# Kernel optimization log

Hardware: AMD Instinct MI355X
Metric: run time of the kernel (lower is better)

The kernel has to match this reference:

```python
import jax, jax.numpy as jnp
import numpy as np

N = 100000
E = 1600000
NFEAT = 128
NHID1 = 128
NHID2 = 128
NCLASS = 40


def setup_inputs() -> dict:
    key = jax.random.key(0)
    ks = jax.random.split(key, 16)
    x = jax.random.normal(ks[0], (N, NFEAT), dtype=jnp.float32)
    src = jax.random.randint(ks[1], (E,), 0, N, dtype=jnp.int32)
    dst = jax.random.randint(ks[2], (E,), 0, N, dtype=jnp.int32)
    s = 0.05
    params = {
        # SAGE layer 1: self branch and neighbor branch
        'w1s': jax.random.normal(ks[3], (NFEAT, NHID1), dtype=jnp.float32) * s,
        'b1s': jnp.zeros((NHID1,), dtype=jnp.float32),
        'w1n': jax.random.normal(ks[4], (NFEAT, NHID1), dtype=jnp.float32) * s,
        'b1n': jnp.zeros((NHID1,), dtype=jnp.float32),
        # SAGE layer 2 (input dim 2*NHID1)
        'w2s': jax.random.normal(ks[5], (2 * NHID1, NHID2), dtype=jnp.float32) * s,
        'b2s': jnp.zeros((NHID2,), dtype=jnp.float32),
        'w2n': jax.random.normal(ks[6], (2 * NHID1, NHID2), dtype=jnp.float32) * s,
        'b2n': jnp.zeros((NHID2,), dtype=jnp.float32),
        # final linear head (input dim 2*NHID2)
        'wfc': jax.random.normal(ks[7], (2 * NHID2, NCLASS), dtype=jnp.float32) * s,
        'bfc': jnp.zeros((NCLASS,), dtype=jnp.float32),
    }
    return {'x': x, 'src': src, 'dst': dst, **params}


def _neigh_mean(h, src, dst, n_nodes):
    # mean aggregation == spmm(row-normalized adj, h), via segment sum over edges
    msg = jax.ops.segment_sum(h[src], dst, num_segments=n_nodes)  # [N, d]
    cnt = jax.ops.segment_sum(jnp.ones((src.shape[0],), h.dtype), dst, num_segments=n_nodes)
    return msg / jnp.maximum(cnt, 1.0)[:, None]


def _sage_layer(h, src, dst, ws, bs, wn, bn):
    neigh = _neigh_mean(h, src, dst, h.shape[0])
    return jnp.concatenate([h @ ws + bs, neigh @ wn + bn], axis=1)


def _l2_normalize(h, eps=1e-12):
    nrm = jnp.sqrt(jnp.sum(h * h, axis=1, keepdims=True))
    return h / jnp.maximum(nrm, eps)


def reference(x, src, dst, w1s, b1s, w1n, b1n, w2s, b2s, w2n, b2n, wfc, bfc):
    h = jax.nn.relu(_sage_layer(x, src, dst, w1s, b1s, w1n, b1n))  # [N, 2*NHID1]
    h = _l2_normalize(h)
    # dropout is identity in eval mode
    h = jax.nn.relu(_sage_layer(h, src, dst, w2s, b2s, w2n, b2n))  # [N, 2*NHID2]
    h = _l2_normalize(h)
    return h @ wfc + bfc  # [N, NCLASS]
```

## Files before the change

### kernel.cpp

```cpp
#include <hip/hip_runtime.h>
#include <hip/hip_bf16.h>


#define N_NODES 100000
#define N_EDGES 1600000
#define NBUCK   196
#define BCAP    12288
#define CHUNK   4096

typedef unsigned short u16;
typedef __bf16 bf16x8 __attribute__((ext_vector_type(8)));
typedef float  f32x4  __attribute__((ext_vector_type(4)));

__device__ __forceinline__ u16 f2b(float f) {
  unsigned x = __builtin_bit_cast(unsigned, f);
  unsigned r = x + 0x7fffu + ((x >> 16) & 1u);
  return (u16)(r >> 16);
}
__device__ __forceinline__ float b2f(u16 u) {
  return __builtin_bit_cast(float, (unsigned)u << 16);
}
__device__ __forceinline__ bf16x8 ldfrag(const u16* p) {
  uint4 u = *reinterpret_cast<const uint4*>(p);
  return __builtin_bit_cast(bf16x8, u);
}

__global__ __launch_bounds__(256) void prep_weights(
    const float* __restrict__ w1s, const float* __restrict__ w1n,
    const float* __restrict__ w2s, const float* __restrict__ w2n,
    const float* __restrict__ wfc,
    u16* __restrict__ WT1, u16* __restrict__ WT2, u16* __restrict__ WFCT) {
  int i = blockIdx.x * 256 + threadIdx.x;
  if (i < 32768) {
    int c = i >> 7, k = i & 127;
    float v = (c < 128) ? w1s[k * 128 + c] : w1n[k * 128 + (c - 128)];
    WT1[c * 128 + k] = f2b(v);
  } else if (i < 32768 + 65536) {
    int j = i - 32768;
    int c = j >> 8, k = j & 255;
    float v = (c < 128) ? w2s[k * 128 + c] : w2n[k * 128 + (c - 128)];
    WT2[c * 256 + k] = f2b(v);
  } else {
    int j = i - 98304;
    int c = j >> 8, k = j & 255;
    float v = (c < 40) ? wfc[k * 40 + c] : 0.f;
    WFCT[c * 256 + k] = f2b(v);
  }
}

__global__ __launch_bounds__(256) void cvt_bf16(const float* __restrict__ x,
                                                u16* __restrict__ xb) {
  size_t i = ((size_t)blockIdx.x * 256 + threadIdx.x) * 8;
  float4 a = *reinterpret_cast<const float4*>(x + i);
  float4 b = *reinterpret_cast<const float4*>(x + i + 4);
  u16 o[8] = {f2b(a.x), f2b(a.y), f2b(a.z), f2b(a.w),
              f2b(b.x), f2b(b.y), f2b(b.z), f2b(b.w)};
  *reinterpret_cast<uint4*>(xb + i) = *reinterpret_cast<const uint4*>(o);
}

__device__ __forceinline__ int wave_incl_scan(int x, int lane) {
#pragma unroll
  for (int d = 1; d < 64; d <<= 1) {
    int n = __shfl_up(x, d, 64);
    if (lane >= d) x += n;
  }
  return x;
}

__global__ __launch_bounds__(256) void bucket_kernel(
    const int* __restrict__ src, const int* __restrict__ dst,
    int* __restrict__ cntg, uint2* __restrict__ pairBuf) {
  __shared__ unsigned hist[NBUCK];
  __shared__ unsigned gbase[NBUCK];
  __shared__ int sws[4];
  __shared__ uint2 stage[CHUNK];
  __shared__ int tgt[CHUNK];
  const int tid = threadIdx.x, lane = tid & 63, wid = tid >> 6;
  const int e0 = blockIdx.x * CHUNK;

  for (int i = tid; i < NBUCK; i += 256) hist[i] = 0u;
  __syncthreads();

  unsigned myD[16], myS[16];
  int myR[16], myB[16];
#pragma unroll
  for (int k = 0; k < 16; ++k) {
    int e = e0 + k * 256 + tid;
    if (e < N_EDGES) {
      unsigned d = (unsigned)dst[e];
      myD[k] = d;
      myS[k] = (unsigned)src[e];
      myB[k] = (int)(d >> 9);
      myR[k] = (int)atomicAdd(&hist[myB[k]], 1u);
    } else {
      myB[k] = -1;
    }
  }
  __syncthreads();

  int cnt = (tid < NBUCK) ? (int)hist[tid] : 0;
  int inc = wave_incl_scan(cnt, lane);
  if (lane == 63) sws[wid] = inc;
  __syncthreads();
  if (wid == 0) {
    int s = (lane < 4) ? sws[lane] : 0;
    s = wave_incl_scan(s, lane);
    if (lane < 4) sws[lane] = s;
  }
  __syncthreads();
  int excl = (wid ? sws[wid - 1] : 0) + inc - cnt;
  int gofs = 0;
  if (tid < NBUCK && cnt > 0) gofs = tid * BCAP + atomicAdd(&cntg[tid], cnt);
  __syncthreads();
  if (tid < NBUCK) {
    hist[tid] = (unsigned)excl;
    gbase[tid] = (unsigned)gofs;
  }
  __syncthreads();

#pragma unroll
  for (int k = 0; k < 16; ++k) {
    if (myB[k] >= 0) {
      int slot = (int)hist[myB[k]] + myR[k];
      uint2 pr;
      pr.x = myD[k];
      pr.y = myS[k];
      stage[slot] = pr;
      tgt[slot] = (int)gbase[myB[k]] + myR[k];
    }
  }
  __syncthreads();
  int nvalid = N_EDGES - e0;
  if (nvalid > CHUNK) nvalid = CHUNK;
  for (int i = tid; i < nvalid; i += 256) pairBuf[tgt[i]] = stage[i];
}

__global__ __launch_bounds__(256) void k_ebase(const int* __restrict__ cntg,
                                               int* __restrict__ ebase) {
  const int tid = threadIdx.x, lane = tid & 63, wid = tid >> 6;
  __shared__ int sws[4];
  int v = (tid < NBUCK) ? cntg[tid] : 0;
  int inc = wave_incl_scan(v, lane);
  if (lane == 63) sws[wid] = inc;
  __syncthreads();
  if (wid == 0) {
    int s = (lane < 4) ? sws[lane] : 0;
    s = wave_incl_scan(s, lane);
    if (lane < 4) sws[lane] = s;
  }
  __syncthreads();
  if (tid < NBUCK) ebase[tid] = (wid ? sws[wid - 1] : 0) + inc - v;
}

__global__ __launch_bounds__(512) void csr_build(
    const uint2* __restrict__ pairBuf, const int* __restrict__ cntg,
    const int* __restrict__ ebase, int* __restrict__ rowptr,
    int* __restrict__ csr) {
  __shared__ int lcnt[512];
  __shared__ int lofs[512];
  __shared__ int sws[8];
  __shared__ int cstage[10240];
  const int b = blockIdx.x, tid = threadIdx.x;
  const int lane = tid & 63, wid = tid >> 6;
  int nb = cntg[b];
  if (nb > BCAP) nb = BCAP;
  if (nb > 10240) nb = 10240;
  const int eb = ebase[b];
  const uint2* pp = pairBuf + (size_t)b * BCAP;

  lcnt[tid] = 0;
  __syncthreads();
  for (int i = tid; i < nb; i += 512) atomicAdd(&lcnt[pp[i].x & 511], 1);
  __syncthreads();
  int v = lcnt[tid];
  int inc = wave_incl_scan(v, lane);
  if (lane == 63) sws[wid] = inc;
  __syncthreads();
  if (wid == 0) {
    int s = (lane < 8) ? sws[lane] : 0;
    s = wave_incl_scan(s, lane);
    if (lane < 8) sws[lane] = s;
  }
  __syncthreads();
  int excl = (wid ? sws[wid - 1] : 0) + inc - v;
  int node = b * 512 + tid;
  if (node <= N_NODES) rowptr[node] = eb + excl;
  lofs[tid] = excl;
  __syncthreads();
  for (int i = tid; i < nb; i += 512) {
    uint2 pr = pp[i];
    int pos = atomicAdd(&lofs[pr.x & 511], 1);
    cstage[pos] = (int)pr.y;
  }
  __syncthreads();
  for (int i = tid; i < nb; i += 512) csr[eb + i] = cstage[i];
}

template <int K>
__global__ __launch_bounds__(256) void gemm_kernel(
    const u16* __restrict__ A, const u16* __restrict__ WT,
    u16* __restrict__ Cs, u16* __restrict__ Cn) {
  constexpr int RB = K * 2;
  constexpr int LOG2RB = (K == 128) ? 8 : 9;
  constexpr int KS = K / 32;
  __shared__ u16 lb[128 * K];

  const int tid = threadIdx.x;
  const int half = blockIdx.x & 1;
  u16* __restrict__ Cout = half ? Cn : Cs;

  const u16* Wsrc = WT + (size_t)half * 128 * K;
  char* lbc = reinterpret_cast<char*>(lb);
#pragma unroll
  for (int i = tid; i < 128 * K / 8; i += 256) {
    uint4 v = *reinterpret_cast<const uint4*>(Wsrc + i * 8);
    int byte = i * 16;
    int swz = byte ^ (((byte >> LOG2RB) & 7) << 4);
    *reinterpret_cast<uint4*>(lbc + swz) = v;
  }
  __syncthreads();

  const int w = tid >> 6, lane = tid & 63;
  const int lrow = lane & 15, lk = lane >> 4;
  const int xr = (lrow & 7) << 4;
  const int stride = gridDim.x >> 1;

  for (int chunk = blockIdx.x >> 1; chunk * 128 < N_NODES; chunk += stride) {
    const int rbase = chunk * 128 + w * 32;
    bf16x8 af[2][KS];
#pragma unroll
    for (int rt = 0; rt < 2; ++rt) {
      int r = rbase + rt * 16 + lrow;
      if (r >= N_NODES) r = N_NODES - 1;
      const u16* ap = A + (size_t)r * K + lk * 8;
#pragma unroll
      for (int ks = 0; ks < KS; ++ks) af[rt][ks] = ldfrag(ap + ks * 32);
    }
    f32x4 acc[2][8];
#pragma unroll
    for (int rt = 0; rt < 2; ++rt)
#pragma unroll
      for (int ct = 0; ct < 8; ++ct) acc[rt][ct] = f32x4{0.f, 0.f, 0.f, 0.f};

#pragma unroll
    for (int ks = 0; ks < KS; ++ks) {
#pragma unroll
      for (int ct = 0; ct < 8; ++ct) {
        int byte = (ct * 16 + lrow) * RB + ks * 64 + lk * 16;
        bf16x8 b = __builtin_bit_cast(
            bf16x8, *reinterpret_cast<const uint4*>(lbc + (byte ^ xr)));
        acc[0][ct] = __builtin_amdgcn_mfma_f32_16x16x32_bf16(af[0][ks], b, acc[0][ct], 0, 0, 0);
        acc[1][ct] = __builtin_amdgcn_mfma_f32_16x16x32_bf16(af[1][ks], b, acc[1][ct], 0, 0, 0);
      }
    }
#pragma unroll
    for (int rt = 0; rt < 2; ++rt) {
#pragma unroll
      for (int j = 0; j < 4; ++j) {
        int r = rbase + rt * 16 + lk * 4 + j;
        if (r < N_NODES) {
          u16* cp = Cout + (size_t)r * 128 + lrow;
#pragma unroll
          for (int ct = 0; ct < 8; ++ct) cp[ct * 16] = f2b(acc[rt][ct][j]);
        }
      }
    }
  }
}

__global__ __launch_bounds__(256) void agg_epi_kernel(
    const u16* __restrict__ Xs, const u16* __restrict__ Xn,
    const int* __restrict__ rowptr, const int* __restrict__ csr,
    const float* __restrict__ bs, const float* __restrict__ bn,
    u16* __restrict__ H) {
  int node = (int)((blockIdx.x * 256 + threadIdx.x) >> 6);
  int lane = threadIdx.x & 63;
  if (node >= N_NODES) return;
  int beg = rowptr[node], end = rowptr[node + 1];
  float a0 = 0.f, a1 = 0.f;
  int j = beg;
  for (; j + 3 < end; j += 4) {
    int s0 = csr[j], s1 = csr[j + 1], s2 = csr[j + 2], s3 = csr[j + 3];
    ushort2 u0 = *reinterpret_cast<const ushort2*>(Xn + (size_t)s0 * 128 + lane * 2);
    ushort2 u1 = *reinterpret_cast<const ushort2*>(Xn + (size_t)s1 * 128 + lane * 2);
    ushort2 u2 = *reinterpret_cast<const ushort2*>(Xn + (size_t)s2 * 128 + lane * 2);
    ushort2 u3 = *reinterpret_cast<const ushort2*>(Xn + (size_t)s3 * 128 + lane * 2);
    a0 += b2f(u0.x) + b2f(u1.x) + b2f(u2.x) + b2f(u3.x);
    a1 += b2f(u0.y) + b2f(u1.y) + b2f(u2.y) + b2f(u3.y);
  }
  for (; j < end; ++j) {
    ushort2 u = *reinterpret_cast<const ushort2*>(Xn + (size_t)csr[j] * 128 + lane * 2);
    a0 += b2f(u.x);
    a1 += b2f(u.y);
  }
  int d = end - beg;
  float inv = 1.f / (float)(d > 0 ? d : 1);
  ushort2 sv = *reinterpret_cast<const ushort2*>(Xs + (size_t)node * 128 + lane * 2);
  float2 bsv = *reinterpret_cast<const float2*>(bs + lane * 2);
  float2 bnv = *reinterpret_cast<const float2*>(bn + lane * 2);
  float s0 = fmaxf(b2f(sv.x) + bsv.x, 0.f);
  float s1 = fmaxf(b2f(sv.y) + bsv.y, 0.f);
  float n0 = fmaxf(a0 * inv + bnv.x, 0.f);
  float n1 = fmaxf(a1 * inv + bnv.y, 0.f);
  float ss = s0 * s0 + s1 * s1 + n0 * n0 + n1 * n1;
#pragma unroll
  for (int off = 1; off < 64; off <<= 1) ss += __shfl_xor(ss, off, 64);
  float sc = 1.f / fmaxf(sqrtf(ss), 1e-12f);
  ushort2 o0, o1;
  o0.x = f2b(s0 * sc);
  o0.y = f2b(s1 * sc);
  o1.x = f2b(n0 * sc);
  o1.y = f2b(n1 * sc);
  *reinterpret_cast<ushort2*>(H + (size_t)node * 256 + lane * 2) = o0;
  *reinterpret_cast<ushort2*>(H + (size_t)node * 256 + 128 + lane * 2) = o1;
}

__global__ __launch_bounds__(256) void fc_kernel(const u16* __restrict__ H2,
                                                 const u16* __restrict__ WFCT,
                                                 const float* __restrict__ bfc,
                                                 float* __restrict__ Out) {
  __shared__ u16 lb[48 * 256];
  char* lbc = reinterpret_cast<char*>(lb);
  const int tid = threadIdx.x;
#pragma unroll
  for (int i = tid; i < 48 * 256 / 8; i += 256) {
    uint4 v = *reinterpret_cast<const uint4*>(WFCT + i * 8);
    int byte = i * 16;
    int swz = byte ^ (((byte >> 9) & 7) << 4);
    *reinterpret_cast<uint4*>(lbc + swz) = v;
  }
  __syncthreads();
  const int w = tid >> 6, lane = tid & 63;
  const int lrow = lane & 15, lk = lane >> 4;
  const int xr = (lrow & 7) << 4;
  const int rbase = blockIdx.x * 64 + w * 16;

  bf16x8 af[8];
  {
    int r = rbase + lrow;
    if (r >= N_NODES) r = N_NODES - 1;
    const u16* ap = H2 + (size_t)r * 256 + lk * 8;
#pragma unroll
    for (int ks = 0; ks < 8; ++ks) af[ks] = ldfrag(ap + ks * 32);
  }
  f32x4 acc[3];
#pragma unroll
  for (int ct = 0; ct < 3; ++ct) acc[ct] = f32x4{0.f, 0.f, 0.f, 0.f};
#pragma unroll
  for (int ks = 0; ks < 8; ++ks) {
#pragma unroll
    for (int ct = 0; ct < 3; ++ct) {
      int byte = (ct * 16 + lrow) * 512 + ks * 64 + lk * 16;
      bf16x8 b = __builtin_bit_cast(
          bf16x8, *reinterpret_cast<const uint4*>(lbc + (byte ^ xr)));
      acc[ct] = __builtin_amdgcn_mfma_f32_16x16x32_bf16(af[ks], b, acc[ct], 0, 0, 0);
    }
  }
#pragma unroll
  for (int j = 0; j < 4; ++j) {
    int r = rbase + lk * 4 + j;
    if (r < N_NODES) {
#pragma unroll
      for (int ct = 0; ct < 3; ++ct) {
        int col = ct * 16 + lrow;
        if (col < 40) Out[(size_t)r * 40 + col] = acc[ct][j] + bfc[col];
      }
    }
  }
}

extern "C" void kernel_launch(void* const* d_in, const int* in_sizes, int n_in,
                              void* d_out, int out_size, void* d_ws, size_t ws_size,
                              hipStream_t stream) {
  const float* x = (const float*)d_in[0];
  const int* src = (const int*)d_in[1];
  const int* dst = (const int*)d_in[2];
  const float* w1s = (const float*)d_in[3];
  const float* b1s = (const float*)d_in[4];
  const float* w1n = (const float*)d_in[5];
  const float* b1n = (const float*)d_in[6];
  const float* w2s = (const float*)d_in[7];
  const float* b2s = (const float*)d_in[8];
  const float* w2n = (const float*)d_in[9];
  const float* b2n = (const float*)d_in[10];
  const float* wfc = (const float*)d_in[11];
  const float* bfc = (const float*)d_in[12];
  float* out = (float*)d_out;

  char* p = (char*)d_ws;
  auto alloc = [&](size_t bytes) {
    char* r = p;
    p += (bytes + 255) & ~(size_t)255;
    return r;
  };
  u16* xb = (u16*)alloc((size_t)N_NODES * 128 * 2);
  u16* XWs = (u16*)alloc((size_t)N_NODES * 128 * 2);
  u16* XWn = (u16*)alloc((size_t)N_NODES * 128 * 2);
  u16* h1 = (u16*)alloc((size_t)N_NODES * 256 * 2);
  u16* WT1 = (u16*)alloc(32768 * 2);
  u16* WT2 = (u16*)alloc(65536 * 2);
  u16* WFCT = (u16*)alloc(12288 * 2);
  uint2* pairBuf = (uint2*)alloc((size_t)NBUCK * BCAP * 8);
  int* cntg = (int*)alloc(NBUCK * 4);
  int* ebase = (int*)alloc(NBUCK * 4);
  int* rowptr = (int*)alloc((N_NODES + 1) * 4);
  int* csr = (int*)alloc((size_t)N_EDGES * 4);
  u16* h2 = h1;

  hipMemsetAsync(cntg, 0, NBUCK * 4, stream);
  prep_weights<<<432, 256, 0, stream>>>(w1s, w1n, w2s, w2n, wfc, WT1, WT2, WFCT);
  cvt_bf16<<<6250, 256, 0, stream>>>(x, xb);
  bucket_kernel<<<391, 256, 0, stream>>>(src, dst, cntg, pairBuf);
  k_ebase<<<1, 256, 0, stream>>>(cntg, ebase);
  csr_build<<<NBUCK, 512, 0, stream>>>(pairBuf, cntg, ebase, rowptr, csr);

  gemm_kernel<128><<<1024, 256, 0, stream>>>(xb, WT1, XWs, XWn);
  agg_epi_kernel<<<25000, 256, 0, stream>>>(XWs, XWn, rowptr, csr, b1s, b1n, h1);
  gemm_kernel<256><<<512, 256, 0, stream>>>(h1, WT2, XWs, XWn);
  agg_epi_kernel<<<25000, 256, 0, stream>>>(XWs, XWn, rowptr, csr, b2s, b2n, h2);
  fc_kernel<<<1563, 256, 0, stream>>>(h2, WFCT, bfc, out);
}
```

Baseline: 387.1 us.

## Fuse fp32 conversion into GEMM, pack edge pairs, vectorize gather, drop scan kernel

Removes the standalone x->bf16 conversion kernel by having the first GEMM load fp32 rows and convert them in registers. Edge (dst-low, src) pairs are packed into one 32-bit word, halving pairBuf traffic. The separate bucket-offset scan kernel is folded into csr_build as a per-block reduction. The aggregation kernel now has 4 edge groups of 16 lanes, each loading 16-byte vectors, then reduces across groups, trading more shuffles for fewer, wider loads. Packing src into 17 bits assumes N < 131072.

```diff
diff --git a/kernel.cpp b/kernel.cpp
--- a/kernel.cpp
+++ b/kernel.cpp
@@ -9,6 +9,7 @@
 #define CHUNK   4096
 
 typedef unsigned short u16;
+typedef unsigned int u32;
 typedef __bf16 bf16x8 __attribute__((ext_vector_type(8)));
 typedef float  f32x4  __attribute__((ext_vector_type(4)));
 
@@ -23,6 +24,24 @@
 __device__ __forceinline__ bf16x8 ldfrag(const u16* p) {
   uint4 u = *reinterpret_cast<const uint4*>(p);
   return __builtin_bit_cast(bf16x8, u);
+}
+__device__ __forceinline__ void unpack8(uint4 u, float* f) {
+  f[0] = __builtin_bit_cast(float, u.x << 16);
+  f[1] = __builtin_bit_cast(float, u.x & 0xffff0000u);
+  f[2] = __builtin_bit_cast(float, u.y << 16);
+  f[3] = __builtin_bit_cast(float, u.y & 0xffff0000u);
+  f[4] = __builtin_bit_cast(float, u.z << 16);
+  f[5] = __builtin_bit_cast(float, u.z & 0xffff0000u);
+  f[6] = __builtin_bit_cast(float, u.w << 16);
+  f[7] = __builtin_bit_cast(float, u.w & 0xffff0000u);
+}
+__device__ __forceinline__ uint4 pack8(const float* f) {
+  uint4 u;
+  u.x = (u32)f2b(f[0]) | ((u32)f2b(f[1]) << 16);
+  u.y = (u32)f2b(f[2]) | ((u32)f2b(f[3]) << 16);
+  u.z = (u32)f2b(f[4]) | ((u32)f2b(f[5]) << 16);
+  u.w = (u32)f2b(f[6]) | ((u32)f2b(f[7]) << 16);
+  return u;
 }
 
 __global__ __launch_bounds__(256) void prep_weights(
@@ -48,16 +67,6 @@
   }
 }
 
-__global__ __launch_bounds__(256) void cvt_bf16(const float* __restrict__ x,
-                                                u16* __restrict__ xb) {
-  size_t i = ((size_t)blockIdx.x * 256 + threadIdx.x) * 8;
-  float4 a = *reinterpret_cast<const float4*>(x + i);
-  float4 b = *reinterpret_cast<const float4*>(x + i + 4);
-  u16 o[8] = {f2b(a.x), f2b(a.y), f2b(a.z), f2b(a.w),
-              f2b(b.x), f2b(b.y), f2b(b.z), f2b(b.w)};
-  *reinterpret_cast<uint4*>(xb + i) = *reinterpret_cast<const uint4*>(o);
-}
-
 __device__ __forceinline__ int wave_incl_scan(int x, int lane) {
 #pragma unroll
   for (int d = 1; d < 64; d <<= 1) {
@@ -69,11 +78,11 @@
 
 __global__ __launch_bounds__(256) void bucket_kernel(
     const int* __restrict__ src, const int* __restrict__ dst,
-    int* __restrict__ cntg, uint2* __restrict__ pairBuf) {
+    int* __restrict__ cntg, u32* __restrict__ pairBuf) {
   __shared__ unsigned hist[NBUCK];
   __shared__ unsigned gbase[NBUCK];
   __shared__ int sws[4];
-  __shared__ uint2 stage[CHUNK];
+  __shared__ u32 stage[CHUNK];
   __shared__ int tgt[CHUNK];
   const int tid = threadIdx.x, lane = tid & 63, wid = tid >> 6;
   const int e0 = blockIdx.x * CHUNK;
@@ -81,15 +90,14 @@
   for (int i = tid; i < NBUCK; i += 256) hist[i] = 0u;
   __syncthreads();
 
-  unsigned myD[16], myS[16];
+  u32 myW[16];
   int myR[16], myB[16];
 #pragma unroll
   for (int k = 0; k < 16; ++k) {
     int e = e0 + k * 256 + tid;
     if (e < N_EDGES) {
       unsigned d = (unsigned)dst[e];
-      myD[k] = d;
-      myS[k] = (unsigned)src[e];
+      myW[k] = ((d & 511u) << 17) | (unsigned)src[e];
       myB[k] = (int)(d >> 9);
       myR[k] = (int)atomicAdd(&hist[myB[k]], 1u);
     } else {
@@ -122,10 +130,7 @@
   for (int k = 0; k < 16; ++k) {
     if (myB[k] >= 0) {
       int slot = (int)hist[myB[k]] + myR[k];
-      uint2 pr;
-      pr.x = myD[k];
-      pr.y = myS[k];
-      stage[slot] = pr;
+      stage[slot] = myW[k];
       tgt[slot] = (int)gbase[myB[k]] + myR[k];
     }
   }
@@ -135,42 +140,41 @@
   for (int i = tid; i < nvalid; i += 256) pairBuf[tgt[i]] = stage[i];
 }
 
-__global__ __launch_bounds__(256) void k_ebase(const int* __restrict__ cntg,
-                                               int* __restrict__ ebase) {
-  const int tid = threadIdx.x, lane = tid & 63, wid = tid >> 6;
-  __shared__ int sws[4];
-  int v = (tid < NBUCK) ? cntg[tid] : 0;
-  int inc = wave_incl_scan(v, lane);
-  if (lane == 63) sws[wid] = inc;
-  __syncthreads();
-  if (wid == 0) {
-    int s = (lane < 4) ? sws[lane] : 0;
-    s = wave_incl_scan(s, lane);
-    if (lane < 4) sws[lane] = s;
-  }
-  __syncthreads();
-  if (tid < NBUCK) ebase[tid] = (wid ? sws[wid - 1] : 0) + inc - v;
-}
-
 __global__ __launch_bounds__(512) void csr_build(
-    const uint2* __restrict__ pairBuf, const int* __restrict__ cntg,
-    const int* __restrict__ ebase, int* __restrict__ rowptr,
-    int* __restrict__ csr) {
+    const u32* __restrict__ pairBuf, const int* __restrict__ cntg,
+    int* __restrict__ rowptr, int* __restrict__ csr) {
   __shared__ int lcnt[512];
   __shared__ int lofs[512];
   __shared__ int sws[8];
+  __shared__ int s_eb;
   __shared__ int cstage[10240];
   const int b = blockIdx.x, tid = threadIdx.x;
   const int lane = tid & 63, wid = tid >> 6;
+
+  {
+    int v = (tid < b) ? cntg[tid] : 0;
+#pragma unroll
+    for (int off = 1; off < 64; off <<= 1) v += __shfl_xor(v, off, 64);
+    if (lane == 0) sws[wid] = v;
+    __syncthreads();
+    if (tid == 0) {
+      int t = 0;
+#pragma unroll
+      for (int i = 0; i < 8; ++i) t += sws[i];
+      s_eb = t;
+    }
+    __syncthreads();
+  }
+  const int eb = s_eb;
   int nb = cntg[b];
   if (nb > BCAP) nb = BCAP;
   if (nb > 10240) nb = 10240;
-  const int eb = ebase[b];
-  const uint2* pp = pairBuf + (size_t)b * BCAP;
+  const u32* pp = pairBuf + (size_t)b * BCAP;
+  __syncthreads();
 
   lcnt[tid] = 0;
   __syncthreads();
-  for (int i = tid; i < nb; i += 512) atomicAdd(&lcnt[pp[i].x & 511], 1);
+  for (int i = tid; i < nb; i += 512) atomicAdd(&lcnt[(pp[i] >> 17) & 511], 1);
   __syncthreads();
   int v = lcnt[tid];
   int inc = wave_incl_scan(v, lane);
@@ -188,17 +192,17 @@
   lofs[tid] = excl;
   __syncthreads();
   for (int i = tid; i < nb; i += 512) {
-    uint2 pr = pp[i];
-    int pos = atomicAdd(&lofs[pr.x & 511], 1);
-    cstage[pos] = (int)pr.y;
+    u32 pr = pp[i];
+    int pos = atomicAdd(&lofs[(pr >> 17) & 511], 1);
+    cstage[pos] = (int)(pr & 0x1FFFFu);
   }
   __syncthreads();
   for (int i = tid; i < nb; i += 512) csr[eb + i] = cstage[i];
 }
 
-template <int K>
+template <int K, bool AF32>
 __global__ __launch_bounds__(256) void gemm_kernel(
-    const u16* __restrict__ A, const u16* __restrict__ WT,
+    const void* __restrict__ Av, const u16* __restrict__ WT,
     u16* __restrict__ Cs, u16* __restrict__ Cn) {
   constexpr int RB = K * 2;
   constexpr int LOG2RB = (K == 128) ? 8 : 9;
@@ -232,9 +236,20 @@
     for (int rt = 0; rt < 2; ++rt) {
       int r = rbase + rt * 16 + lrow;
       if (r >= N_NODES) r = N_NODES - 1;
-      const u16* ap = A + (size_t)r * K + lk * 8;
-#pragma unroll
-      for (int ks = 0; ks < KS; ++ks) af[rt][ks] = ldfrag(ap + ks * 32);
+      if constexpr (AF32) {
+        const float* ap = (const float*)Av + (size_t)r * K + lk * 8;
+#pragma unroll
+        for (int ks = 0; ks < KS; ++ks) {
+          float4 f0 = *reinterpret_cast<const float4*>(ap + ks * 32);
+          float4 f1 = *reinterpret_cast<const float4*>(ap + ks * 32 + 4);
+          float f[8] = {f0.x, f0.y, f0.z, f0.w, f1.x, f1.y, f1.z, f1.w};
+          af[rt][ks] = __builtin_bit_cast(bf16x8, pack8(f));
+        }
+      } else {
+        const u16* ap = (const u16*)Av + (size_t)r * K + lk * 8;
+#pragma unroll
+        for (int ks = 0; ks < KS; ++ks) af[rt][ks] = ldfrag(ap + ks * 32);
+      }
     }
     f32x4 acc[2][8];
 #pragma unroll
@@ -276,43 +291,63 @@
   int node = (int)((blockIdx.x * 256 + threadIdx.x) >> 6);
   int lane = threadIdx.x & 63;
   if (node >= N_NODES) return;
+  const int g = lane >> 4;
+  const int lc = lane & 15;
   int beg = rowptr[node], end = rowptr[node + 1];
-  float a0 = 0.f, a1 = 0.f;
-  int j = beg;
-  for (; j + 3 < end; j += 4) {
-    int s0 = csr[j], s1 = csr[j + 1], s2 = csr[j + 2], s3 = csr[j + 3];
-    ushort2 u0 = *reinterpret_cast<const ushort2*>(Xn + (size_t)s0 * 128 + lane * 2);
-    ushort2 u1 = *reinterpret_cast<const ushort2*>(Xn + (size_t)s1 * 128 + lane * 2);
-    ushort2 u2 = *reinterpret_cast<const ushort2*>(Xn + (size_t)s2 * 128 + lane * 2);
-    ushort2 u3 = *reinterpret_cast<const ushort2*>(Xn + (size_t)s3 * 128 + lane * 2);
-    a0 += b2f(u0.x) + b2f(u1.x) + b2f(u2.x) + b2f(u3.x);
-    a1 += b2f(u0.y) + b2f(u1.y) + b2f(u2.y) + b2f(u3.y);
-  }
-  for (; j < end; ++j) {
-    ushort2 u = *reinterpret_cast<const ushort2*>(Xn + (size_t)csr[j] * 128 + lane * 2);
-    a0 += b2f(u.x);
-    a1 += b2f(u.y);
+
+  float acc[8] = {0.f, 0.f, 0.f, 0.f, 0.f, 0.f, 0.f, 0.f};
+  const u16* colbase = Xn + lc * 8;
+  for (int j = beg; j < end; j += 4) {
+    int e = j + g;
+    int s = (e < end) ? csr[e] : 0;
+    uint4 u = *reinterpret_cast<const uint4*>(colbase + (size_t)s * 128);
+    if (e < end) {
+      float f[8];
+      unpack8(u, f);
+#pragma unroll
+      for (int i = 0; i < 8; ++i) acc[i] += f[i];
+    }
+  }
+#pragma unroll
+  for (int i = 0; i < 8; ++i) {
+    acc[i] += __shfl_xor(acc[i], 32, 64);
+    acc[i] += __shfl_xor(acc[i], 16, 64);
   }
   int d = end - beg;
   float inv = 1.f / (float)(d > 0 ? d : 1);
-  ushort2 sv = *reinterpret_cast<const ushort2*>(Xs + (size_t)node * 128 + lane * 2);
-  float2 bsv = *reinterpret_cast<const float2*>(bs + lane * 2);
-  float2 bnv = *reinterpret_cast<const float2*>(bn + lane * 2);
-  float s0 = fmaxf(b2f(sv.x) + bsv.x, 0.f);
-  float s1 = fmaxf(b2f(sv.y) + bsv.y, 0.f);
-  float n0 = fmaxf(a0 * inv + bnv.x, 0.f);
-  float n1 = fmaxf(a1 * inv + bnv.y, 0.f);
-  float ss = s0 * s0 + s1 * s1 + n0 * n0 + n1 * n1;
-#pragma unroll
-  for (int off = 1; off < 64; off <<= 1) ss += __shfl_xor(ss, off, 64);
+
+  uint4 sv4 = *reinterpret_cast<const uint4*>(Xs + (size_t)node * 128 + lc * 8);
+  float sf[8];
+  unpack8(sv4, sf);
+  float4 b0 = *reinterpret_cast<const float4*>(bs + lc * 8);
+  float4 b1 = *reinterpret_cast<const float4*>(bs + lc * 8 + 4);
+  float4 c0 = *reinterpret_cast<const float4*>(bn + lc * 8);
+  float4 c1 = *reinterpret_cast<const float4*>(bn + lc * 8 + 4);
+  float bsv[8] = {b0.x, b0.y, b0.z, b0.w, b1.x, b1.y, b1.z, b1.w};
+  float bnv[8] = {c0.x, c0.y, c0.z, c0.w, c1.x, c1.y, c1.z, c1.w};
+  float nf[8];
+  float ss = 0.f;
+#pragma unroll
+  for (int i = 0; i < 8; ++i) {
+    sf[i] = fmaxf(sf[i] + bsv[i], 0.f);
+    nf[i] = fmaxf(acc[i] * inv + bnv[i], 0.f);
+    ss += sf[i] * sf[i] + nf[i] * nf[i];
+  }
+  ss += __shfl_xor(ss, 1, 64);
+  ss += __shfl_xor(ss, 2, 64);
+  ss += __shfl_xor(ss, 4, 64);
+  ss += __shfl_xor(ss, 8, 64);
   float sc = 1.f / fmaxf(sqrtf(ss), 1e-12f);
-  ushort2 o0, o1;
-  o0.x = f2b(s0 * sc);
-  o0.y = f2b(s1 * sc);
-  o1.x = f2b(n0 * sc);
-  o1.y = f2b(n1 * sc);
-  *reinterpret_cast<ushort2*>(H + (size_t)node * 256 + lane * 2) = o0;
-  *reinterpret_cast<ushort2*>(H + (size_t)node * 256 + 128 + lane * 2) = o1;
+#pragma unroll
+  for (int i = 0; i < 8; ++i) {
+    sf[i] *= sc;
+    nf[i] *= sc;
+  }
+  if (g == 0) {
+    *reinterpret_cast<uint4*>(H + (size_t)node * 256 + lc * 8) = pack8(sf);
+  } else if (g == 1) {
+    *reinterpret_cast<uint4*>(H + (size_t)node * 256 + 128 + lc * 8) = pack8(nf);
+  }
 }
 
 __global__ __launch_bounds__(256) void fc_kernel(const u16* __restrict__ H2,
@@ -393,30 +428,26 @@
     p += (bytes + 255) & ~(size_t)255;
     return r;
   };
-  u16* xb = (u16*)alloc((size_t)N_NODES * 128 * 2);
   u16* XWs = (u16*)alloc((size_t)N_NODES * 128 * 2);
   u16* XWn = (u16*)alloc((size_t)N_NODES * 128 * 2);
   u16* h1 = (u16*)alloc((size_t)N_NODES * 256 * 2);
   u16* WT1 = (u16*)alloc(32768 * 2);
   u16* WT2 = (u16*)alloc(65536 * 2);
   u16* WFCT = (u16*)alloc(12288 * 2);
-  uint2* pairBuf = (uint2*)alloc((size_t)NBUCK * BCAP * 8);
+  u32* pairBuf = (u32*)alloc((size_t)NBUCK * BCAP * 4);
   int* cntg = (int*)alloc(NBUCK * 4);
-  int* ebase = (int*)alloc(NBUCK * 4);
   int* rowptr = (int*)alloc((N_NODES + 1) * 4);
   int* csr = (int*)alloc((size_t)N_EDGES * 4);
   u16* h2 = h1;
 
   hipMemsetAsync(cntg, 0, NBUCK * 4, stream);
   prep_weights<<<432, 256, 0, stream>>>(w1s, w1n, w2s, w2n, wfc, WT1, WT2, WFCT);
-  cvt_bf16<<<6250, 256, 0, stream>>>(x, xb);
   bucket_kernel<<<391, 256, 0, stream>>>(src, dst, cntg, pairBuf);
-  k_ebase<<<1, 256, 0, stream>>>(cntg, ebase);
-  csr_build<<<NBUCK, 512, 0, stream>>>(pairBuf, cntg, ebase, rowptr, csr);
-
-  gemm_kernel<128><<<1024, 256, 0, stream>>>(xb, WT1, XWs, XWn);
+  csr_build<<<NBUCK, 512, 0, stream>>>(pairBuf, cntg, rowptr, csr);
+
+  gemm_kernel<128, true><<<1024, 256, 0, stream>>>(x, WT1, XWs, XWn);
   agg_epi_kernel<<<25000, 256, 0, stream>>>(XWs, XWn, rowptr, csr, b1s, b1n, h1);
-  gemm_kernel<256><<<512, 256, 0, stream>>>(h1, WT2, XWs, XWn);
+  gemm_kernel<256, false><<<512, 256, 0, stream>>>(h1, WT2, XWs, XWn);
   agg_epi_kernel<<<25000, 256, 0, stream>>>(XWs, XWn, rowptr, csr, b2s, b2n, h2);
   fc_kernel<<<1563, 256, 0, stream>>>(h2, WFCT, bfc, out);
 }
```

After: 386.1 us. About the same (-0.3%).
